# Kernel tuning notes

Measured on AMD Instinct MI355X. Metric: run time of the kernel, lower is better.

Reference implementation:

```python
import jax, jax.numpy as jnp
import numpy as np

B, T, D, H = 4, 4096, 4096, 128  # head_size = embedding_size // num_heads = 4096 // 32

def setup_inputs() -> dict:
    key = jax.random.key(0)
    kx, kq, kk, kv = jax.random.split(key, 4)
    x = jax.random.normal(kx, (B, T, D), dtype=jnp.float32)
    # Dense kernels (no bias), init scale 0.01 as in the module
    Wq = jax.random.normal(kq, (D, H), dtype=jnp.float32) * 0.01
    Wk = jax.random.normal(kk, (D, H), dtype=jnp.float32) * 0.01
    Wv = jax.random.normal(kv, (D, H), dtype=jnp.float32) * 0.01
    return {"x": x, "Wq": Wq, "Wk": Wk, "Wv": Wv}

def reference(x, Wq, Wk, Wv):
    # Single-head projections: (B,T,D) @ (D,H) -> (B,T,H)
    Q = jnp.einsum('btd,dh->bth', x, Wq)
    K = jnp.einsum('btd,dh->bth', x, Wk)
    V = jnp.einsum('btd,dh->bth', x, Wv)
    scale = 1.0 / jnp.sqrt(jnp.asarray(H, dtype=Q.dtype))
    scores = jnp.einsum('bth,bsh->bts', Q, K) * scale  # (B,T,S) full score matrix
    weights = jax.nn.softmax(scores, axis=-1)
    # dropout rate = 0.0 (deterministic/eval) -> identity
    out = jnp.einsum('bts,bsh->bth', weights, V)  # (B,T,H)
    return out
```

## Files before the change

### kernel.cpp

```cpp
#include <hip/hip_runtime.h>


typedef __bf16 bf16_t;
typedef bf16_t bf16x8 __attribute__((ext_vector_type(8)));
typedef float f32x4 __attribute__((ext_vector_type(4)));
typedef float f32x8 __attribute__((ext_vector_type(8)));

#define MFMA16(A, B, C) __builtin_amdgcn_mfma_f32_16x16x32_bf16((A), (B), (C), 0, 0, 0)

__device__ __forceinline__ void async_cp16(const bf16_t* g, bf16_t* lds) {
  __builtin_amdgcn_global_load_lds(
      (__attribute__((address_space(1))) unsigned int*)g,
      (__attribute__((address_space(3))) unsigned int*)lds, 16, 0, 0);
}

__global__ void tr_w(const float* __restrict__ w0, const float* __restrict__ w1,
                     const float* __restrict__ w2, bf16_t* __restrict__ wt) {
  __shared__ float tile[32][33];
  const int z = blockIdx.z;
  const float* src = (z == 0) ? w0 : (z == 1) ? w1 : w2;
  bf16_t* dst = wt + (size_t)z * 128 * 4096;
  const int c0 = blockIdx.x * 32;
  const int r0 = blockIdx.y * 32;
  const int tx = threadIdx.x, ty = threadIdx.y;
#pragma unroll
  for (int j = 0; j < 4; ++j)
    tile[ty + 8 * j][tx] = src[(size_t)(r0 + ty + 8 * j) * 128 + c0 + tx];
  __syncthreads();
#pragma unroll
  for (int j = 0; j < 4; ++j)
    dst[(size_t)(c0 + ty + 8 * j) * 4096 + r0 + tx] = (bf16_t)tile[tx][ty + 8 * j];
}

__global__ void tr_v(const bf16_t* __restrict__ v, bf16_t* __restrict__ vt) {
  __shared__ bf16_t tile[32][33];
  const int b = blockIdx.z;
  const bf16_t* src = v + (size_t)b * 4096 * 128;
  bf16_t* dst = vt + (size_t)b * 128 * 4096;
  const int c0 = blockIdx.x * 32;
  const int r0 = blockIdx.y * 32;
  const int tx = threadIdx.x, ty = threadIdx.y;
#pragma unroll
  for (int j = 0; j < 4; ++j)
    tile[ty + 8 * j][tx] = src[(size_t)(r0 + ty + 8 * j) * 128 + c0 + tx];
  __syncthreads();
#pragma unroll
  for (int j = 0; j < 4; ++j)
    dst[(size_t)(c0 + ty + 8 * j) * 4096 + r0 + tx] = tile[tx][ty + 8 * j];
}

__device__ __forceinline__ void stage_b(const bf16_t* __restrict__ wt_k,
                                        bf16_t* sBbuf, int tid) {
#pragma unroll
  for (int r = 0; r < 6; ++r) {
    int cid = r * 256 + tid;
    int n = cid >> 3, pc = cid & 7;
    int lc = pc ^ (n & 7);
    async_cp16(wt_k + (size_t)n * 4096 + lc * 8, sBbuf + (size_t)cid * 8);
  }
}

__launch_bounds__(256, 2)
__global__ void qkv_proj(const float* __restrict__ x, const bf16_t* __restrict__ wt,
                         bf16_t* __restrict__ q, bf16_t* __restrict__ k,
                         bf16_t* __restrict__ v) {
  __shared__ __align__(16) bf16_t sA[2][64 * 64];
  __shared__ __align__(16) bf16_t sB[2][192 * 64];
  const int tid = threadIdx.x;
  const int w = tid >> 6, lane = tid & 63, lq = lane & 15, quad = lane >> 4;
  const int wr = w >> 1, wc = w & 1;
  const int m0 = (int)(blockIdx.x >> 1) * 64;
  const int nb = (int)(blockIdx.x & 1) * 192;
  const bf16_t* wtb = wt + (size_t)nb * 4096;

  int arow[2], apc[2], alc[2];
#pragma unroll
  for (int r = 0; r < 2; ++r) {
    int ca = r * 256 + tid;
    arow[r] = ca >> 3;
    apc[r] = ca & 7;
    alc[r] = apc[r] ^ (arow[r] & 7);
  }
  const float* xb = x + (size_t)m0 * 4096;

  f32x4 acc[2][6];
#pragma unroll
  for (int i = 0; i < 2; ++i)
#pragma unroll
    for (int j = 0; j < 6; ++j) acc[i][j] = (f32x4){0.f, 0.f, 0.f, 0.f};

  float4 fA[4];
#pragma unroll
  for (int r = 0; r < 2; ++r) {
    const float4* p = (const float4*)(xb + (size_t)arow[r] * 4096 + alc[r] * 8);
    fA[2 * r] = p[0];
    fA[2 * r + 1] = p[1];
  }
  stage_b(wtb, sB[0], tid);
#pragma unroll
  for (int r = 0; r < 2; ++r) {
    f32x8 ff = {fA[2 * r].x, fA[2 * r].y, fA[2 * r].z, fA[2 * r].w,
                fA[2 * r + 1].x, fA[2 * r + 1].y, fA[2 * r + 1].z, fA[2 * r + 1].w};
    *(bf16x8*)(sA[0] + arow[r] * 64 + apc[r] * 8) = __builtin_convertvector(ff, bf16x8);
  }
#pragma unroll
  for (int r = 0; r < 2; ++r) {
    const float4* p = (const float4*)(xb + (size_t)arow[r] * 4096 + 64 + alc[r] * 8);
    fA[2 * r] = p[0];
    fA[2 * r + 1] = p[1];
  }
  asm volatile("s_waitcnt vmcnt(4) lgkmcnt(0)" ::: "memory");
  __builtin_amdgcn_s_barrier();

  for (int kt = 0; kt < 64; ++kt) {
    const int buf = kt & 1;
    const int ktB = (kt < 63) ? kt + 1 : 63;
    stage_b(wtb + ktB * 64, sB[buf ^ 1], tid);
#pragma unroll
    for (int r = 0; r < 2; ++r) {
      f32x8 ff = {fA[2 * r].x, fA[2 * r].y, fA[2 * r].z, fA[2 * r].w,
                  fA[2 * r + 1].x, fA[2 * r + 1].y, fA[2 * r + 1].z, fA[2 * r + 1].w};
      *(bf16x8*)(sA[buf ^ 1] + arow[r] * 64 + apc[r] * 8) =
          __builtin_convertvector(ff, bf16x8);
    }
    const int ktA = (kt < 62) ? kt + 2 : 63;
#pragma unroll
    for (int r = 0; r < 2; ++r) {
      const float4* p =
          (const float4*)(xb + (size_t)arow[r] * 4096 + ktA * 64 + alc[r] * 8);
      fA[2 * r] = p[0];
      fA[2 * r + 1] = p[1];
    }
#pragma unroll
    for (int ks = 0; ks < 2; ++ks) {
      bf16x8 af[2], bfr[6];
      const int cc = ks * 4 + quad;
#pragma unroll
      for (int mt = 0; mt < 2; ++mt) {
        int row = wr * 32 + mt * 16 + lq;
        af[mt] = *(const bf16x8*)(sA[buf] + row * 64 + ((cc ^ (row & 7)) << 3));
      }
#pragma unroll
      for (int nt = 0; nt < 6; ++nt) {
        int n = wc * 96 + nt * 16 + lq;
        bfr[nt] = *(const bf16x8*)(sB[buf] + n * 64 + ((cc ^ (n & 7)) << 3));
      }
#pragma unroll
      for (int mt = 0; mt < 2; ++mt)
#pragma unroll
        for (int nt = 0; nt < 6; ++nt) acc[mt][nt] = MFMA16(af[mt], bfr[nt], acc[mt][nt]);
    }
    asm volatile("s_waitcnt vmcnt(4) lgkmcnt(0)" ::: "memory");
    __builtin_amdgcn_s_barrier();
  }
#pragma unroll
  for (int mt = 0; mt < 2; ++mt) {
#pragma unroll
    for (int nt = 0; nt < 6; ++nt) {
      int n = nb + wc * 96 + nt * 16 + lq;
      bf16_t* dst;
      int nn;
      if (n < 128) { dst = q; nn = n; }
      else if (n < 256) { dst = k; nn = n - 128; }
      else { dst = v; nn = n - 256; }
#pragma unroll
      for (int r = 0; r < 4; ++r) {
        int m = m0 + wr * 32 + mt * 16 + quad * 4 + r;
        dst[(size_t)m * 128 + nn] = (bf16_t)acc[mt][nt][r];
      }
    }
  }
}

__device__ __forceinline__ void stage_kv(const bf16_t* __restrict__ ksrc,
                                         const bf16_t* __restrict__ vsrc,
                                         bf16_t* sKbuf, bf16_t* sVbuf, int tid) {
#pragma unroll
  for (int r = 0; r < 4; ++r) {
    int cid = r * 256 + tid;
    int row = cid >> 4, pc = cid & 15;
    int lc = pc ^ (row & 15);
    async_cp16(ksrc + row * 128 + lc * 8, sKbuf + (size_t)cid * 8);
  }
#pragma unroll
  for (int r = 0; r < 4; ++r) {
    int cid = r * 256 + tid;
    int h = cid >> 3, pc = cid & 7;
    int lc = pc ^ (h & 7);
    async_cp16(vsrc + (size_t)h * 4096 + lc * 8, sVbuf + (size_t)cid * 8);
  }
}

__launch_bounds__(256, 2)
__global__ void flash(const bf16_t* __restrict__ q, const bf16_t* __restrict__ kk,
                      const bf16_t* __restrict__ vt, float* __restrict__ opart,
                      float* __restrict__ mlm, float* __restrict__ mll) {
  __shared__ __align__(16) bf16_t sK[2][64 * 128];
  __shared__ __align__(16) bf16_t sV[2][128 * 64];
  __shared__ __align__(16) bf16_t sP[64 * 72];
  const int tid = threadIdx.x;
  const int w = tid >> 6, lane = tid & 63, lq = lane & 15, quad = lane >> 4;
  const int b = blockIdx.x & 3;
  const int qt = (blockIdx.x >> 2) & 63;
  const int sp = blockIdx.x >> 8;
  const int qrow0 = qt * 64;

  bf16x8 qf[4];
  {
    const bf16_t* qp = q + ((size_t)b * 4096 + qrow0 + w * 16 + lq) * 128 + quad * 8;
#pragma unroll
    for (int ks = 0; ks < 4; ++ks) qf[ks] = *(const bf16x8*)(qp + ks * 32);
  }

  f32x4 accO[8];
#pragma unroll
  for (int i = 0; i < 8; ++i) accO[i] = (f32x4){0.f, 0.f, 0.f, 0.f};
  float mrow[4] = {-1e30f, -1e30f, -1e30f, -1e30f};
  float lrow[4] = {0.f, 0.f, 0.f, 0.f};

  const bf16_t* kbase = kk + (size_t)b * 4096 * 128;
  const bf16_t* vbase = vt + (size_t)b * 128 * 4096;
  const float SCL = 0.08838834764831845f * 1.4426950408889634f;
  const int it0 = sp * 32;

  stage_kv(kbase + (size_t)it0 * 64 * 128, vbase + it0 * 64, sK[0], sV[0], tid);
  __syncthreads();

  for (int i = 0; i < 32; ++i) {
    const int buf = i & 1;
    if (i < 31)
      stage_kv(kbase + (size_t)(it0 + i + 1) * 64 * 128, vbase + (it0 + i + 1) * 64,
               sK[buf ^ 1], sV[buf ^ 1], tid);

    f32x4 accS[4];
#pragma unroll
    for (int nt = 0; nt < 4; ++nt) accS[nt] = (f32x4){0.f, 0.f, 0.f, 0.f};
    __builtin_amdgcn_s_setprio(1);
#pragma unroll
    for (int ks = 0; ks < 4; ++ks) {
      const int cc = ks * 4 + quad;
#pragma unroll
      for (int nt = 0; nt < 4; ++nt) {
        int row = nt * 16 + lq;
        bf16x8 kf = *(const bf16x8*)(sK[buf] + row * 128 + ((cc ^ (row & 15)) << 3));
        accS[nt] = MFMA16(qf[ks], kf, accS[nt]);
      }
    }
    __builtin_amdgcn_s_setprio(0);

    float mxs[4];
#pragma unroll
    for (int r = 0; r < 4; ++r) {
      float t0 = fmaxf(fmaxf(accS[0][r], accS[1][r]), fmaxf(accS[2][r], accS[3][r]));
#pragma unroll
      for (int msk = 1; msk < 16; msk <<= 1) t0 = fmaxf(t0, __shfl_xor(t0, msk));
      mxs[r] = t0 * SCL;
    }
    bool grow = (mxs[0] > mrow[0]) || (mxs[1] > mrow[1]) ||
                (mxs[2] > mrow[2]) || (mxs[3] > mrow[3]);
    if (__any(grow)) {
      float al[4];
#pragma unroll
      for (int r = 0; r < 4; ++r) {
        float mn = fmaxf(mrow[r], mxs[r]);
        al[r] = exp2f(mrow[r] - mn);
        mrow[r] = mn;
        lrow[r] *= al[r];
      }
#pragma unroll
      for (int ot = 0; ot < 8; ++ot) {
        accO[ot][0] *= al[0]; accO[ot][1] *= al[1];
        accO[ot][2] *= al[2]; accO[ot][3] *= al[3];
      }
    }
    float ps[4] = {0.f, 0.f, 0.f, 0.f};
#pragma unroll
    for (int nt = 0; nt < 4; ++nt)
#pragma unroll
      for (int r = 0; r < 4; ++r) {
        float p = exp2f(fmaf(accS[nt][r], SCL, -mrow[r]));
        accS[nt][r] = p;
        ps[r] += p;
      }
#pragma unroll
    for (int r = 0; r < 4; ++r) {
      float s = ps[r];
#pragma unroll
      for (int msk = 1; msk < 16; msk <<= 1) s += __shfl_xor(s, msk);
      lrow[r] += s;
    }

#pragma unroll
    for (int nt = 0; nt < 4; ++nt) {
      int key = nt * 16 + lq;
#pragma unroll
      for (int r = 0; r < 4; ++r) {
        int prow = w * 16 + quad * 4 + r;
        sP[prow * 72 + key] = (bf16_t)accS[nt][r];
      }
    }

    __builtin_amdgcn_s_setprio(1);
#pragma unroll
    for (int ks2 = 0; ks2 < 2; ++ks2) {
      const int cc = ks2 * 4 + quad;
      bf16x8 pf = *(const bf16x8*)(sP + (w * 16 + lq) * 72 + cc * 8);
#pragma unroll
      for (int ot = 0; ot < 8; ++ot) {
        int h = ot * 16 + lq;
        bf16x8 vf = *(const bf16x8*)(sV[buf] + h * 64 + ((cc ^ (h & 7)) << 3));
        accO[ot] = MFMA16(pf, vf, accO[ot]);
      }
    }
    __builtin_amdgcn_s_setprio(0);
    __syncthreads();
  }

  float* op = opart + ((size_t)(sp * 4 + b) * 4096 + qrow0 + w * 16) * 128;
#pragma unroll
  for (int ot = 0; ot < 8; ++ot)
#pragma unroll
    for (int r = 0; r < 4; ++r)
      op[(size_t)(quad * 4 + r) * 128 + ot * 16 + lq] = accO[ot][r];
  if (lq == 0) {
#pragma unroll
    for (int r = 0; r < 4; ++r) {
      size_t idx = (size_t)(sp * 4 + b) * 4096 + qrow0 + w * 16 + quad * 4 + r;
      mlm[idx] = mrow[r];
      mll[idx] = lrow[r];
    }
  }
}

__global__ void merge(const float* __restrict__ opart, const float* __restrict__ mlm,
                      const float* __restrict__ mll, float* __restrict__ out) {
  const int idx = blockIdx.x * 256 + threadIdx.x;
  const int h = idx & 127;
  const int row = idx >> 7;
  float m0 = mlm[row], m1 = mlm[16384 + row];
  float l0 = mll[row], l1 = mll[16384 + row];
  float M = fmaxf(m0, m1);
  float w0 = exp2f(m0 - M), w1 = exp2f(m1 - M);
  float L = w0 * l0 + w1 * l1;
  float acc = w0 * opart[(size_t)row * 128 + h] +
              w1 * opart[((size_t)16384 + row) * 128 + h];
  out[idx] = acc / L;
}

extern "C" void kernel_launch(void* const* d_in, const int* in_sizes, int n_in,
                              void* d_out, int out_size, void* d_ws, size_t ws_size,
                              hipStream_t stream) {
  (void)in_sizes; (void)n_in; (void)out_size; (void)ws_size;
  const float* x  = (const float*)d_in[0];
  const float* wq = (const float*)d_in[1];
  const float* wk = (const float*)d_in[2];
  const float* wv = (const float*)d_in[3];

  char* ws = (char*)d_ws;
  bf16_t* wt  = (bf16_t*)ws;                         ws += (size_t)384 * 4096 * 2;
  bf16_t* qb  = (bf16_t*)ws;                         ws += (size_t)16384 * 128 * 2;
  bf16_t* kb  = (bf16_t*)ws;                         ws += (size_t)16384 * 128 * 2;
  bf16_t* vb  = (bf16_t*)ws;                         ws += (size_t)16384 * 128 * 2;
  bf16_t* vtb = (bf16_t*)ws;                         ws += (size_t)16384 * 128 * 2;
  float*  opart = (float*)ws;                        ws += (size_t)2 * 16384 * 128 * 4;
  float*  mlm = (float*)ws;                          ws += (size_t)2 * 16384 * 4;
  float*  mll = (float*)ws;
  float*  ob  = (float*)d_out;

  dim3 tb(32, 8, 1);
  tr_w<<<dim3(4, 128, 3), tb, 0, stream>>>(wq, wk, wv, wt);
  qkv_proj<<<dim3(512), dim3(256), 0, stream>>>(x, wt, qb, kb, vb);
  tr_v<<<dim3(4, 128, 4), tb, 0, stream>>>(vb, vtb);
  flash<<<dim3(512), dim3(256), 0, stream>>>(qb, kb, vtb, opart, mlm, mll);
  merge<<<dim3(8192), dim3(256), 0, stream>>>(opart, mlm, mll, ob);
}
```

Measured before the change: 513.8 us.

## Shrink projection and flash tiles to raise occupancy across both kernels

The QKV projection now gives each block a 64x128 output tile (one of Q, K or V) instead of 64x192. That raises the grid to 768 blocks, lowers LDS and accumulator use, and allows three blocks per CU. The flash kernel halves its key tile to 32 rows and now runs 64 iterations per split, which cuts LDS so four blocks fit per CU. The cost is more loop iterations, more barriers and softmax reductions per key, and x being re-read three times in the projection. Scheduling barriers are also added around the load stages of the projection.

```diff
diff --git a/kernel.cpp b/kernel.cpp
--- a/kernel.cpp
+++ b/kernel.cpp
@@ -52,7 +52,7 @@
 __device__ __forceinline__ void stage_b(const bf16_t* __restrict__ wt_k,
                                         bf16_t* sBbuf, int tid) {
 #pragma unroll
-  for (int r = 0; r < 6; ++r) {
+  for (int r = 0; r < 4; ++r) {
     int cid = r * 256 + tid;
     int n = cid >> 3, pc = cid & 7;
     int lc = pc ^ (n & 7);
@@ -60,18 +60,19 @@
   }
 }
 
-__launch_bounds__(256, 2)
+__launch_bounds__(256, 3)
 __global__ void qkv_proj(const float* __restrict__ x, const bf16_t* __restrict__ wt,
                          bf16_t* __restrict__ q, bf16_t* __restrict__ k,
                          bf16_t* __restrict__ v) {
   __shared__ __align__(16) bf16_t sA[2][64 * 64];
-  __shared__ __align__(16) bf16_t sB[2][192 * 64];
+  __shared__ __align__(16) bf16_t sB[2][128 * 64];
   const int tid = threadIdx.x;
   const int w = tid >> 6, lane = tid & 63, lq = lane & 15, quad = lane >> 4;
   const int wr = w >> 1, wc = w & 1;
-  const int m0 = (int)(blockIdx.x >> 1) * 64;
-  const int nb = (int)(blockIdx.x & 1) * 192;
-  const bf16_t* wtb = wt + (size_t)nb * 4096;
+  const int mblk = (int)blockIdx.x / 3;
+  const int nblk = (int)blockIdx.x - mblk * 3;
+  const int m0 = mblk * 64;
+  const bf16_t* wtb = wt + (size_t)nblk * 128 * 4096;
 
   int arow[2], apc[2], alc[2];
 #pragma unroll
@@ -83,32 +84,33 @@
   }
   const float* xb = x + (size_t)m0 * 4096;
 
-  f32x4 acc[2][6];
+  f32x4 acc[2][4];
 #pragma unroll
   for (int i = 0; i < 2; ++i)
 #pragma unroll
-    for (int j = 0; j < 6; ++j) acc[i][j] = (f32x4){0.f, 0.f, 0.f, 0.f};
+    for (int j = 0; j < 4; ++j) acc[i][j] = (f32x4){0.f, 0.f, 0.f, 0.f};
 
   float4 fA[4];
-#pragma unroll
-  for (int r = 0; r < 2; ++r) {
-    const float4* p = (const float4*)(xb + (size_t)arow[r] * 4096 + alc[r] * 8);
-    fA[2 * r] = p[0];
-    fA[2 * r + 1] = p[1];
-  }
+#define LOADA(KT)                                                              \
+  {                                                                            \
+    _Pragma("unroll") for (int r = 0; r < 2; ++r) {                            \
+      const float4* p =                                                        \
+          (const float4*)(xb + (size_t)arow[r] * 4096 + (KT)*64 + alc[r] * 8); \
+      fA[2 * r] = p[0];                                                        \
+      fA[2 * r + 1] = p[1];                                                    \
+    }                                                                          \
+  }
+
+  LOADA(0);
   stage_b(wtb, sB[0], tid);
+  __builtin_amdgcn_sched_barrier(0);
 #pragma unroll
   for (int r = 0; r < 2; ++r) {
     f32x8 ff = {fA[2 * r].x, fA[2 * r].y, fA[2 * r].z, fA[2 * r].w,
                 fA[2 * r + 1].x, fA[2 * r + 1].y, fA[2 * r + 1].z, fA[2 * r + 1].w};
     *(bf16x8*)(sA[0] + arow[r] * 64 + apc[r] * 8) = __builtin_convertvector(ff, bf16x8);
   }
-#pragma unroll
-  for (int r = 0; r < 2; ++r) {
-    const float4* p = (const float4*)(xb + (size_t)arow[r] * 4096 + 64 + alc[r] * 8);
-    fA[2 * r] = p[0];
-    fA[2 * r + 1] = p[1];
-  }
+  LOADA(1);
   asm volatile("s_waitcnt vmcnt(4) lgkmcnt(0)" ::: "memory");
   __builtin_amdgcn_s_barrier();
 
@@ -116,6 +118,7 @@
     const int buf = kt & 1;
     const int ktB = (kt < 63) ? kt + 1 : 63;
     stage_b(wtb + ktB * 64, sB[buf ^ 1], tid);
+    __builtin_amdgcn_sched_barrier(0);
 #pragma unroll
     for (int r = 0; r < 2; ++r) {
       f32x8 ff = {fA[2 * r].x, fA[2 * r].y, fA[2 * r].z, fA[2 * r].w,
@@ -124,16 +127,11 @@
           __builtin_convertvector(ff, bf16x8);
     }
     const int ktA = (kt < 62) ? kt + 2 : 63;
-#pragma unroll
-    for (int r = 0; r < 2; ++r) {
-      const float4* p =
-          (const float4*)(xb + (size_t)arow[r] * 4096 + ktA * 64 + alc[r] * 8);
-      fA[2 * r] = p[0];
-      fA[2 * r + 1] = p[1];
-    }
+    LOADA(ktA);
+    __builtin_amdgcn_sched_barrier(0);
 #pragma unroll
     for (int ks = 0; ks < 2; ++ks) {
-      bf16x8 af[2], bfr[6];
+      bf16x8 af[2], bfr[4];
       const int cc = ks * 4 + quad;
 #pragma unroll
       for (int mt = 0; mt < 2; ++mt) {
@@ -141,28 +139,26 @@
         af[mt] = *(const bf16x8*)(sA[buf] + row * 64 + ((cc ^ (row & 7)) << 3));
       }
 #pragma unroll
-      for (int nt = 0; nt < 6; ++nt) {
-        int n = wc * 96 + nt * 16 + lq;
+      for (int nt = 0; nt < 4; ++nt) {
+        int n = wc * 64 + nt * 16 + lq;
         bfr[nt] = *(const bf16x8*)(sB[buf] + n * 64 + ((cc ^ (n & 7)) << 3));
       }
 #pragma unroll
       for (int mt = 0; mt < 2; ++mt)
 #pragma unroll
-        for (int nt = 0; nt < 6; ++nt) acc[mt][nt] = MFMA16(af[mt], bfr[nt], acc[mt][nt]);
+        for (int nt = 0; nt < 4; ++nt) acc[mt][nt] = MFMA16(af[mt], bfr[nt], acc[mt][nt]);
     }
     asm volatile("s_waitcnt vmcnt(4) lgkmcnt(0)" ::: "memory");
     __builtin_amdgcn_s_barrier();
   }
+#undef LOADA
+
+  bf16_t* dst = (nblk == 0) ? q : (nblk == 1) ? k : v;
 #pragma unroll
   for (int mt = 0; mt < 2; ++mt) {
 #pragma unroll
-    for (int nt = 0; nt < 6; ++nt) {
-      int n = nb + wc * 96 + nt * 16 + lq;
-      bf16_t* dst;
-      int nn;
-      if (n < 128) { dst = q; nn = n; }
-      else if (n < 256) { dst = k; nn = n - 128; }
-      else { dst = v; nn = n - 256; }
+    for (int nt = 0; nt < 4; ++nt) {
+      int nn = wc * 64 + nt * 16 + lq;
 #pragma unroll
       for (int r = 0; r < 4; ++r) {
         int m = m0 + wr * 32 + mt * 16 + quad * 4 + r;
@@ -176,28 +172,28 @@
                                          const bf16_t* __restrict__ vsrc,
                                          bf16_t* sKbuf, bf16_t* sVbuf, int tid) {
 #pragma unroll
-  for (int r = 0; r < 4; ++r) {
+  for (int r = 0; r < 2; ++r) {
     int cid = r * 256 + tid;
     int row = cid >> 4, pc = cid & 15;
     int lc = pc ^ (row & 15);
     async_cp16(ksrc + row * 128 + lc * 8, sKbuf + (size_t)cid * 8);
   }
 #pragma unroll
-  for (int r = 0; r < 4; ++r) {
+  for (int r = 0; r < 2; ++r) {
     int cid = r * 256 + tid;
-    int h = cid >> 3, pc = cid & 7;
-    int lc = pc ^ (h & 7);
+    int h = cid >> 2, pc = cid & 3;
+    int lc = pc ^ (h & 3);
     async_cp16(vsrc + (size_t)h * 4096 + lc * 8, sVbuf + (size_t)cid * 8);
   }
 }
 
-__launch_bounds__(256, 2)
+__launch_bounds__(256, 4)
 __global__ void flash(const bf16_t* __restrict__ q, const bf16_t* __restrict__ kk,
                       const bf16_t* __restrict__ vt, float* __restrict__ opart,
                       float* __restrict__ mlm, float* __restrict__ mll) {
-  __shared__ __align__(16) bf16_t sK[2][64 * 128];
-  __shared__ __align__(16) bf16_t sV[2][128 * 64];
-  __shared__ __align__(16) bf16_t sP[64 * 72];
+  __shared__ __align__(16) bf16_t sK[2][32 * 128];
+  __shared__ __align__(16) bf16_t sV[2][128 * 32];
+  __shared__ __align__(16) bf16_t sP[64 * 40];
   const int tid = threadIdx.x;
   const int w = tid >> 6, lane = tid & 63, lq = lane & 15, quad = lane >> 4;
   const int b = blockIdx.x & 3;
@@ -221,26 +217,26 @@
   const bf16_t* kbase = kk + (size_t)b * 4096 * 128;
   const bf16_t* vbase = vt + (size_t)b * 128 * 4096;
   const float SCL = 0.08838834764831845f * 1.4426950408889634f;
-  const int it0 = sp * 32;
-
-  stage_kv(kbase + (size_t)it0 * 64 * 128, vbase + it0 * 64, sK[0], sV[0], tid);
+  const int it0 = sp * 64;
+
+  stage_kv(kbase + (size_t)it0 * 32 * 128, vbase + it0 * 32, sK[0], sV[0], tid);
   __syncthreads();
 
-  for (int i = 0; i < 32; ++i) {
+  for (int i = 0; i < 64; ++i) {
     const int buf = i & 1;
-    if (i < 31)
-      stage_kv(kbase + (size_t)(it0 + i + 1) * 64 * 128, vbase + (it0 + i + 1) * 64,
+    if (i < 63)
+      stage_kv(kbase + (size_t)(it0 + i + 1) * 32 * 128, vbase + (it0 + i + 1) * 32,
                sK[buf ^ 1], sV[buf ^ 1], tid);
 
-    f32x4 accS[4];
-#pragma unroll
-    for (int nt = 0; nt < 4; ++nt) accS[nt] = (f32x4){0.f, 0.f, 0.f, 0.f};
+    f32x4 accS[2];
+#pragma unroll
+    for (int nt = 0; nt < 2; ++nt) accS[nt] = (f32x4){0.f, 0.f, 0.f, 0.f};
     __builtin_amdgcn_s_setprio(1);
 #pragma unroll
     for (int ks = 0; ks < 4; ++ks) {
       const int cc = ks * 4 + quad;
 #pragma unroll
-      for (int nt = 0; nt < 4; ++nt) {
+      for (int nt = 0; nt < 2; ++nt) {
         int row = nt * 16 + lq;
         bf16x8 kf = *(const bf16x8*)(sK[buf] + row * 128 + ((cc ^ (row & 15)) << 3));
         accS[nt] = MFMA16(qf[ks], kf, accS[nt]);
@@ -251,7 +247,7 @@
     float mxs[4];
 #pragma unroll
     for (int r = 0; r < 4; ++r) {
-      float t0 = fmaxf(fmaxf(accS[0][r], accS[1][r]), fmaxf(accS[2][r], accS[3][r]));
+      float t0 = fmaxf(accS[0][r], accS[1][r]);
 #pragma unroll
       for (int msk = 1; msk < 16; msk <<= 1) t0 = fmaxf(t0, __shfl_xor(t0, msk));
       mxs[r] = t0 * SCL;
@@ -275,7 +271,7 @@
     }
     float ps[4] = {0.f, 0.f, 0.f, 0.f};
 #pragma unroll
-    for (int nt = 0; nt < 4; ++nt)
+    for (int nt = 0; nt < 2; ++nt)
 #pragma unroll
       for (int r = 0; r < 4; ++r) {
         float p = exp2f(fmaf(accS[nt][r], SCL, -mrow[r]));
@@ -291,24 +287,22 @@
     }
 
 #pragma unroll
-    for (int nt = 0; nt < 4; ++nt) {
+    for (int nt = 0; nt < 2; ++nt) {
       int key = nt * 16 + lq;
 #pragma unroll
       for (int r = 0; r < 4; ++r) {
         int prow = w * 16 + quad * 4 + r;
-        sP[prow * 72 + key] = (bf16_t)accS[nt][r];
+        sP[prow * 40 + key] = (bf16_t)accS[nt][r];
       }
     }
 
     __builtin_amdgcn_s_setprio(1);
-#pragma unroll
-    for (int ks2 = 0; ks2 < 2; ++ks2) {
-      const int cc = ks2 * 4 + quad;
-      bf16x8 pf = *(const bf16x8*)(sP + (w * 16 + lq) * 72 + cc * 8);
+    {
+      bf16x8 pf = *(const bf16x8*)(sP + (w * 16 + lq) * 40 + quad * 8);
 #pragma unroll
       for (int ot = 0; ot < 8; ++ot) {
         int h = ot * 16 + lq;
-        bf16x8 vf = *(const bf16x8*)(sV[buf] + h * 64 + ((cc ^ (h & 7)) << 3));
+        bf16x8 vf = *(const bf16x8*)(sV[buf] + h * 32 + ((quad ^ (h & 3)) << 3));
         accO[ot] = MFMA16(pf, vf, accO[ot]);
       }
     }
@@ -369,7 +363,7 @@
 
   dim3 tb(32, 8, 1);
   tr_w<<<dim3(4, 128, 3), tb, 0, stream>>>(wq, wk, wv, wt);
-  qkv_proj<<<dim3(512), dim3(256), 0, stream>>>(x, wt, qb, kb, vb);
+  qkv_proj<<<dim3(768), dim3(256), 0, stream>>>(x, wt, qb, kb, vb);
   tr_v<<<dim3(4, 128, 4), tb, 0, stream>>>(vb, vtb);
   flash<<<dim3(512), dim3(256), 0, stream>>>(qb, kb, vtb, opart, mlm, mll);
   merge<<<dim3(8192), dim3(256), 0, stream>>>(opart, mlm, mll, ob);
```

Result: slower. 536.8 us (+4.5%).
